# Performance work log

Hardware: AMD Instinct MI355X
Metric: run time of the kernel (lower is better)

Reference implementation:

```python
import jax, jax.numpy as jnp
import numpy as np

N = 50000          # num_nodes
IN_CH = 128
H = 32             # hidden_channels
D = 2              # stalk dimension d (= final_d, add_lp=add_hp=False)
LAYERS = 4
EU = 400000        # undirected edges
E = 2 * EU         # directed edges (both orientations)
OUT = 32


def setup_inputs() -> dict:
    key = jax.random.key(0)
    ks = jax.random.split(key, 12)
    # undirected random graph; directed edge list holds both orientations so that
    # the reverse of directed edge e is e + EU (mod E)
    u = jax.random.randint(ks[0], (EU,), 0, N)
    v = jax.random.randint(ks[1], (EU,), 0, N)
    edge_index = jnp.stack([jnp.concatenate([u, v]), jnp.concatenate([v, u])]).astype(jnp.int64)
    x = jax.random.normal(ks[2], (N, IN_CH), dtype=jnp.float32)
    W1 = jax.random.normal(ks[3], (H * D, IN_CH), dtype=jnp.float32) / np.sqrt(IN_CH)
    b1 = jax.random.normal(ks[4], (H * D,), dtype=jnp.float32) * 0.01
    W_sheaf = jax.random.normal(ks[5], (LAYERS, D, 2 * D * H), dtype=jnp.float32) / np.sqrt(2 * D * H)
    # lin_left initialised to identity in the module; keep near-identity
    W_left = jnp.tile(jnp.eye(D, dtype=jnp.float32), (LAYERS, 1, 1)) \
        + 0.01 * jax.random.normal(ks[6], (LAYERS, D, D), dtype=jnp.float32)
    W_right = jax.random.normal(ks[7], (LAYERS, H, H), dtype=jnp.float32) / np.sqrt(H)
    eps = jnp.zeros((LAYERS, D, 1), dtype=jnp.float32) + 0.01 * jax.random.normal(ks[8], (LAYERS, D, 1), dtype=jnp.float32)
    W2 = jax.random.normal(ks[9], (OUT, D * H), dtype=jnp.float32) / np.sqrt(D * H)
    b2 = jax.random.normal(ks[10], (OUT,), dtype=jnp.float32) * 0.01
    return {"x": x, "edge_index": edge_index, "W1": W1, "b1": b1, "W_sheaf": W_sheaf,
            "W_left": W_left, "W_right": W_right, "eps": eps, "W2": W2, "b2": b2}


def reference(x, edge_index, W1, b1, W_sheaf, W_left, W_right, eps, W2, b2):
    # eval mode: dropouts are no-ops; diagnostic energies/eigsh omitted (no effect on output)
    n = x.shape[0]
    d = W_left.shape[-1]
    h = W_right.shape[-1]
    src, dst = edge_index[0], edge_index[1]
    e = src.shape[0]
    rev = (jnp.arange(e) + e // 2) % e  # reverse directed edge

    x = jax.nn.elu(x @ W1.T + b1)      # [N, d*h]
    x = x.reshape(n * d, h)
    x0 = x

    for l in range(W_left.shape[0]):
        # --- sheaf learner: tanh(Linear([x_i || x_j])), diag maps F: [E, d] ---
        xn = x.reshape(n, d * h)
        feat = jnp.concatenate([xn[src], xn[dst]], axis=-1)   # [E, 2dh]
        F = jnp.tanh(feat @ W_sheaf[l].T)                     # [E, d]
        Fr = F[rev]
        # --- diag sheaf Laplacian (normalised, augmented: D_hat = D + I) ---
        Dg = jax.ops.segment_sum(F * F, src, num_segments=n)  # [N, d] diagonal blocks
        dinv = jax.lax.rsqrt(Dg + 1.0)
        diagw = Dg * dinv * dinv                              # [N, d]
        offw = -F * Fr * dinv[src] * dinv[dst]                # [E, d]
        # --- left weights: view x^T as [h, N, d], mix stalk dim ---
        xt = x.T.reshape(h, n, d) @ W_left[l].T
        x = xt.reshape(h, n * d).T
        # --- right weights ---
        x = x @ W_right[l].T
        # --- spmm: y = L x ---
        x3 = x.reshape(n, d, h)
        y = diagw[:, :, None] * x3 \
            + jax.ops.segment_sum(offw[:, :, None] * x3[dst], src, num_segments=n)
        x = jax.nn.elu(y.reshape(n * d, h))
        # --- epsilon-gated residual ---
        coeff = jnp.tile(1.0 + jnp.tanh(eps[l]), (n, 1))      # [N*d, 1]
        x0 = coeff * x0 - x
        x = x0

    return x.reshape(n, d * h) @ W2.T + b2
```

## Files before the change

kernel.cpp:

```cpp
#include <hip/hip_runtime.h>
#include <math.h>

#define INCH 128
#define DH 64
#define H  32
#define D  2
#define LAYERS 4
#define OUTC 32

typedef __fp16 half4 __attribute__((ext_vector_type(4)));
typedef float  f32x4 __attribute__((ext_vector_type(4)));

__device__ __forceinline__ float eluf(float v) { return v > 0.f ? v : expm1f(v); }

__device__ __forceinline__ float ftanh(float x) {
    float xc = fminf(9.0f, fmaxf(-9.0f, x));
    float e2 = __builtin_amdgcn_exp2f(xc * 2.885390081777927f);
    return (e2 - 1.0f) * __builtin_amdgcn_rcpf(e2 + 1.0f);
}

__global__ void k_prep(const float* __restrict__ W1, const float* __restrict__ W2,
                       const float* __restrict__ Wleft, const float* __restrict__ Wright,
                       __fp16* __restrict__ W1h, __fp16* __restrict__ W2h,
                       __fp16* __restrict__ Mlrh) {
    int idx = blockIdx.x * blockDim.x + threadIdx.x;
    if (idx < DH * INCH) {
        W1h[idx] = (__fp16)W1[idx];
    } else if (idx < DH * INCH + OUTC * DH) {
        int i = idx - DH * INCH;
        W2h[i] = (__fp16)W2[i];
    } else if (idx < DH * INCH + OUTC * DH + LAYERS * DH * DH) {
        int i = idx - DH * INCH - OUTC * DH;
        int l = i >> 12;
        int r = i & 4095;
        int row = r >> 6;
        int col = r & 63;
        int sp = row >> 5, c = row & 31;
        int s  = col >> 5, cp = col & 31;
        Mlrh[i] = (__fp16)(Wleft[l * 4 + sp * 2 + s] * Wright[l * 1024 + c * 32 + cp]);
    }
}

__global__ void k_hist(const int* __restrict__ src, int* __restrict__ deg, int E) {
    int e = blockIdx.x * blockDim.x + threadIdx.x;
    if (e < E) atomicAdd(&deg[src[e]], 1);
}

__global__ void k_bsum(const int* __restrict__ deg, int* __restrict__ bsum, int N) {
    int b = blockIdx.x, t = threadIdx.x;
    int lane = t & 63, wid = t >> 6;
    int base = b * 1024 + t * 4;
    int s = 0;
    #pragma unroll
    for (int i = 0; i < 4; ++i) {
        int idx = base + i;
        if (idx < N) s += deg[idx];
    }
    #pragma unroll
    for (int ofs = 32; ofs; ofs >>= 1) s += __shfl_xor(s, ofs);
    __shared__ int ws[4];
    if (lane == 0) ws[wid] = s;
    __syncthreads();
    if (t == 0) bsum[b] = ws[0] + ws[1] + ws[2] + ws[3];
}

__global__ void k_scan_small(int* __restrict__ bsum, int B) {
    int lane = threadIdx.x;
    int carry = 0;
    for (int base = 0; base < B; base += 64) {
        int i = base + lane;
        int v = (i < B) ? bsum[i] : 0;
        int incl = v;
        #pragma unroll
        for (int ofs = 1; ofs < 64; ofs <<= 1) {
            int tt = __shfl_up(incl, ofs);
            if (lane >= ofs) incl += tt;
        }
        if (i < B) bsum[i] = carry + incl - v;
        carry += __shfl(incl, 63);
    }
}

__global__ void k_scan_final(const int* __restrict__ deg, const int* __restrict__ bsum,
                             int* __restrict__ rowptr, int* __restrict__ cur, int N) {
    int b = blockIdx.x, t = threadIdx.x;
    int lane = t & 63, wid = t >> 6;
    int base = b * 1024 + t * 4;
    int v[4];
    int s = 0;
    #pragma unroll
    for (int i = 0; i < 4; ++i) {
        int idx = base + i;
        v[i] = (idx < N) ? deg[idx] : 0;
        s += v[i];
    }
    int incl = s;
    #pragma unroll
    for (int ofs = 1; ofs < 64; ofs <<= 1) {
        int tt = __shfl_up(incl, ofs);
        if (lane >= ofs) incl += tt;
    }
    __shared__ int ws[4];
    if (lane == 63) ws[wid] = incl;
    __syncthreads();
    int woff = 0;
    for (int k = 0; k < wid; ++k) woff += ws[k];
    int excl = bsum[b] + woff + incl - s;
    #pragma unroll
    for (int i = 0; i < 4; ++i) {
        int idx = base + i;
        if (idx < N) { rowptr[idx] = excl; cur[idx] = excl; }
        excl += v[i];
        if (idx == N - 1) rowptr[N] = excl;
    }
}

__global__ void k_scatter(const int* __restrict__ src, const int* __restrict__ dst,
                          int* __restrict__ cur, int* __restrict__ csr_dst, int E) {
    int e = blockIdx.x * blockDim.x + threadIdx.x;
    if (e >= E) return;
    int pos = atomicAdd(&cur[src[e]], 1);
    csr_dst[pos] = dst[e];
}


__global__ __launch_bounds__(256) void k_mlp1(const float* __restrict__ xin,
                                              const __fp16* __restrict__ W1h,
                                              const float* __restrict__ b1,
                                              float* __restrict__ X, int N) {
    __shared__ float xs[16 * INCH];
    __shared__ __fp16 wsh[DH * 132];
    int t = threadIdx.x;
    int node0 = blockIdx.x * 16;
    for (int i = t; i < 16 * INCH / 4; i += 256) {
        int r = i >> 5, c = (i & 31) * 4;
        int node = node0 + r;
        f32x4 v = (node < N) ? __builtin_nontemporal_load((const f32x4*)(xin + (size_t)node * INCH + c))
                             : (f32x4){0.f, 0.f, 0.f, 0.f};
        *(f32x4*)&xs[r * INCH + c] = v;
    }
    for (int i = t; i < DH * INCH / 4; i += 256) {
        int r = i >> 5, c = (i & 31) * 4;
        *(uint2*)&wsh[r * 132 + c] = ((const uint2*)W1h)[i];
    }
    __syncthreads();
    int w = t >> 6, lane = t & 63;
    int oc0 = w * 16;
    int rr = lane & 15, g = lane >> 4;
    f32x4 acc = {0.f, 0.f, 0.f, 0.f};
    #pragma unroll
    for (int ks = 0; ks < INCH / 16; ++ks) {
        f32x4 xv = *(const f32x4*)&xs[rr * INCH + ks * 16 + g * 4];
        half4 af = {(__fp16)xv.x, (__fp16)xv.y, (__fp16)xv.z, (__fp16)xv.w};
        half4 bf = *(const half4*)&wsh[(oc0 + rr) * 132 + ks * 16 + g * 4];
        acc = __builtin_amdgcn_mfma_f32_16x16x16f16(af, bf, acc, 0, 0, 0);
    }
    int oc = oc0 + rr;
    float bb = b1[oc];
    #pragma unroll
    for (int r = 0; r < 4; ++r) {
        int node = node0 + g * 4 + r;
        if (node < N) X[(size_t)node * DH + oc] = eluf(acc[r] + bb);
    }
}

__global__ void k_pq(const float* __restrict__ X, const float* __restrict__ Wsl,
                     float4* __restrict__ PQ4, int N) {
    int wid = (blockIdx.x * blockDim.x + threadIdx.x) >> 6;
    int lane = threadIdx.x & 63;
    if (wid >= N) return;
    float x = X[(size_t)wid * DH + lane];
    float p0 = x * Wsl[lane];
    float q0 = x * Wsl[64 + lane];
    float p1 = x * Wsl[128 + lane];
    float q1 = x * Wsl[192 + lane];
    #pragma unroll
    for (int ofs = 32; ofs; ofs >>= 1) {
        p0 += __shfl_xor(p0, ofs);
        q0 += __shfl_xor(q0, ofs);
        p1 += __shfl_xor(p1, ofs);
        q1 += __shfl_xor(q1, ofs);
    }
    if (lane == 0) PQ4[wid] = make_float4(p0, p1, q0, q1);
}

__global__ __launch_bounds__(256) void k_lr(const float* __restrict__ X,
                                            const __fp16* __restrict__ Mlrh_l,
                                            __fp16* __restrict__ XW0h,
                                            __fp16* __restrict__ XW1h, int N) {
    __shared__ float xs[16 * DH];
    __shared__ __fp16 mlh[DH * 68];
    int t = threadIdx.x;
    int node0 = blockIdx.x * 16;
    for (int i = t; i < 16 * DH / 4; i += 256) {
        int r = i >> 4, c = (i & 15) * 4;
        int node = node0 + r;
        f32x4 v = (node < N) ? __builtin_nontemporal_load((const f32x4*)(X + (size_t)node * DH + c))
                             : (f32x4){0.f, 0.f, 0.f, 0.f};
        *(f32x4*)&xs[r * DH + c] = v;
    }
    for (int i = t; i < DH * DH / 4; i += 256) {
        int r = i >> 4, c = (i & 15) * 4;
        *(uint2*)&mlh[r * 68 + c] = ((const uint2*)Mlrh_l)[i];
    }
    __syncthreads();
    int w = t >> 6, lane = t & 63;
    int oc0 = w * 16;
    int rr = lane & 15, g = lane >> 4;
    f32x4 acc = {0.f, 0.f, 0.f, 0.f};
    #pragma unroll
    for (int ks = 0; ks < DH / 16; ++ks) {
        f32x4 xv = *(const f32x4*)&xs[rr * DH + ks * 16 + g * 4];
        half4 af = {(__fp16)xv.x, (__fp16)xv.y, (__fp16)xv.z, (__fp16)xv.w};
        half4 bf = *(const half4*)&mlh[(oc0 + rr) * 68 + ks * 16 + g * 4];
        acc = __builtin_amdgcn_mfma_f32_16x16x16f16(af, bf, acc, 0, 0, 0);
    }
    int oc = oc0 + rr;
    int sp = oc >> 5, c = oc & 31;
    __fp16* __restrict__ XWs = sp ? XW1h : XW0h;
    #pragma unroll
    for (int r = 0; r < 4; ++r) {
        int node = node0 + g * 4 + r;
        if (node < N) XWs[(size_t)node * H + c] = (__fp16)acc[r];
    }
}

__global__ __launch_bounds__(256) void k_out(const float* __restrict__ X,
                                             const __fp16* __restrict__ W2h,
                                             const float* __restrict__ b2,
                                             float* __restrict__ out, int N) {
    __shared__ float xs[32 * DH];
    __shared__ __fp16 w2s[OUTC * 68];
    int t = threadIdx.x;
    int node0 = blockIdx.x * 32;
    for (int i = t; i < 32 * DH / 4; i += 256) {
        int r = i >> 4, c = (i & 15) * 4;
        int node = node0 + r;
        f32x4 v = (node < N) ? __builtin_nontemporal_load((const f32x4*)(X + (size_t)node * DH + c))
                             : (f32x4){0.f, 0.f, 0.f, 0.f};
        *(f32x4*)&xs[r * DH + c] = v;
    }
    for (int i = t; i < OUTC * DH / 4; i += 256) {
        int r = i >> 4, c = (i & 15) * 4;
        *(uint2*)&w2s[r * 68 + c] = ((const uint2*)W2h)[i];
    }
    __syncthreads();
    int w = t >> 6, lane = t & 63;
    int nt = w >> 1;
    int oc0 = (w & 1) * 16;
    int rr = lane & 15, g = lane >> 4;
    f32x4 acc = {0.f, 0.f, 0.f, 0.f};
    #pragma unroll
    for (int ks = 0; ks < DH / 16; ++ks) {
        f32x4 xv = *(const f32x4*)&xs[(nt * 16 + rr) * DH + ks * 16 + g * 4];
        half4 af = {(__fp16)xv.x, (__fp16)xv.y, (__fp16)xv.z, (__fp16)xv.w};
        half4 bf = *(const half4*)&w2s[(oc0 + rr) * 68 + ks * 16 + g * 4];
        acc = __builtin_amdgcn_mfma_f32_16x16x16f16(af, bf, acc, 0, 0, 0);
    }
    int oc = oc0 + rr;
    float bb = b2[oc];
    #pragma unroll
    for (int r = 0; r < 4; ++r) {
        int node = node0 + nt * 16 + g * 4 + r;
        if (node < N) out[(size_t)node * OUTC + oc] = acc[r] + bb;
    }
}


__global__ void k_dg(const float4* __restrict__ PQ4, const int* __restrict__ rowptr,
                     const int* __restrict__ csr_dst, float4* __restrict__ DGI, int N) {
    int wid = (blockIdx.x * blockDim.x + threadIdx.x) >> 6;
    int lane = threadIdx.x & 63;
    int nn = lane >> 4, sub = lane & 15;
    int node = wid * 4 + nn;
    if (node >= N) return;
    float4 pqu = PQ4[node];
    int pos = rowptr[node], end = rowptr[node + 1];
    float sx = 0.f, sy = 0.f;
    for (int i = pos + sub; i < end; i += 16) {
        int v = __builtin_nontemporal_load(csr_dst + i);
        float4 pqv = PQ4[v];
        float fx = ftanh(pqu.x + pqv.z);
        float fy = ftanh(pqu.y + pqv.w);
        sx += fx * fx;
        sy += fy * fy;
    }
    #pragma unroll
    for (int ofs = 8; ofs; ofs >>= 1) {
        sx += __shfl_xor(sx, ofs);
        sy += __shfl_xor(sy, ofs);
    }
    if (sub == 0) {
        float i0 = 1.f / (sx + 1.f), i1 = 1.f / (sy + 1.f);
        DGI[node] = make_float4(sqrtf(i0), sqrtf(i1), sx * i0, sy * i1);
    }
}

__global__ void k_spmm_fin_pq(const __fp16* __restrict__ XW0h, const __fp16* __restrict__ XW1h,
                              const float4* __restrict__ PQ4, const int* __restrict__ rowptr,
                              const int* __restrict__ csr_dst, const float4* __restrict__ DGI,
                              const float* __restrict__ eps_l, const float* __restrict__ Wsn,
                              float* __restrict__ X, float4* __restrict__ PQ4n, int N) {
    int wid = (blockIdx.x * blockDim.x + threadIdx.x) >> 6;
    int lane = threadIdx.x & 63;
    if (wid >= N) return;
    int q = lane >> 3;
    int m = lane & 7;
    float4 pqu = PQ4[wid];
    float4 giu = DGI[wid];
    float dinv0 = giu.x, dinv1 = giu.y;
    int pos = rowptr[wid], end = rowptr[wid + 1];

    float a0x = 0.f, a0y = 0.f, a0z = 0.f, a0w = 0.f;
    float a1x = 0.f, a1y = 0.f, a1z = 0.f, a1w = 0.f;

    for (int chunk = pos; chunk < end; chunk += 64) {
        int myidx = chunk + lane;
        int dmy = 0;
        float w0my = 0.f, w1my = 0.f;
        if (myidx < end) {
            dmy = __builtin_nontemporal_load(csr_dst + myidx);
            float4 pqd = PQ4[dmy];
            float4 gid = DGI[dmy];
            float ff0 = ftanh(pqu.x + pqd.z), fb0 = ftanh(pqd.x + pqu.z);
            float ff1 = ftanh(pqu.y + pqd.w), fb1 = ftanh(pqd.y + pqu.w);
            w0my = -ff0 * fb0 * dinv0 * gid.x;
            w1my = -ff1 * fb1 * dinv1 * gid.y;
        }
        int lim = end - chunk; if (lim > 64) lim = 64;
        for (int b = 0; b < lim; b += 8) {
            int sl = b + q;
            int d      = __shfl(dmy, sl);
            float w0e  = __shfl(w0my, sl);
            float w1e  = __shfl(w1my, sl);
            half4 g0 = *(const half4*)(XW0h + (size_t)d * H + m * 4);
            half4 g1 = *(const half4*)(XW1h + (size_t)d * H + m * 4);
            a0x += w0e * (float)g0.x; a0y += w0e * (float)g0.y;
            a0z += w0e * (float)g0.z; a0w += w0e * (float)g0.w;
            a1x += w1e * (float)g1.x; a1y += w1e * (float)g1.y;
            a1z += w1e * (float)g1.z; a1w += w1e * (float)g1.w;
        }
    }
    #pragma unroll
    for (int ofs = 8; ofs <= 32; ofs <<= 1) {
        a0x += __shfl_xor(a0x, ofs); a0y += __shfl_xor(a0y, ofs);
        a0z += __shfl_xor(a0z, ofs); a0w += __shfl_xor(a0w, ofs);
        a1x += __shfl_xor(a1x, ofs); a1y += __shfl_xor(a1y, ofs);
        a1z += __shfl_xor(a1z, ofs); a1w += __shfl_xor(a1w, ofs);
    }
    if (q == 0) {
        float diag0 = giu.z;
        float diag1 = giu.w;
        half4 xw0 = *(const half4*)(XW0h + (size_t)wid * H + m * 4);
        half4 xw1 = *(const half4*)(XW1h + (size_t)wid * H + m * 4);
        size_t b0 = (size_t)wid * DH + m * 4;
        size_t b1 = b0 + 32;
        float coeff0 = 1.f + tanhf(eps_l[0]);
        float coeff1 = 1.f + tanhf(eps_l[1]);
        f32x4 xo0 = __builtin_nontemporal_load((const f32x4*)(X + b0));
        f32x4 xo1 = __builtin_nontemporal_load((const f32x4*)(X + b1));
        f32x4 xn0, xn1;
        xn0.x = coeff0 * xo0.x - eluf(diag0 * (float)xw0.x + a0x);
        xn0.y = coeff0 * xo0.y - eluf(diag0 * (float)xw0.y + a0y);
        xn0.z = coeff0 * xo0.z - eluf(diag0 * (float)xw0.z + a0z);
        xn0.w = coeff0 * xo0.w - eluf(diag0 * (float)xw0.w + a0w);
        xn1.x = coeff1 * xo1.x - eluf(diag1 * (float)xw1.x + a1x);
        xn1.y = coeff1 * xo1.y - eluf(diag1 * (float)xw1.y + a1y);
        xn1.z = coeff1 * xo1.z - eluf(diag1 * (float)xw1.z + a1z);
        xn1.w = coeff1 * xo1.w - eluf(diag1 * (float)xw1.w + a1w);
        __builtin_nontemporal_store(xn0, (f32x4*)(X + b0));
        __builtin_nontemporal_store(xn1, (f32x4*)(X + b1));
        if (Wsn) {
            f32x4 wa0 = *(const f32x4*)(Wsn + m * 4);
            f32x4 wa1 = *(const f32x4*)(Wsn + 32 + m * 4);
            f32x4 wb0 = *(const f32x4*)(Wsn + 64 + m * 4);
            f32x4 wb1 = *(const f32x4*)(Wsn + 96 + m * 4);
            f32x4 wc0 = *(const f32x4*)(Wsn + 128 + m * 4);
            f32x4 wc1 = *(const f32x4*)(Wsn + 160 + m * 4);
            f32x4 wd0 = *(const f32x4*)(Wsn + 192 + m * 4);
            f32x4 wd1 = *(const f32x4*)(Wsn + 224 + m * 4);
            float p0 = xn0.x * wa0.x + xn0.y * wa0.y + xn0.z * wa0.z + xn0.w * wa0.w
                     + xn1.x * wa1.x + xn1.y * wa1.y + xn1.z * wa1.z + xn1.w * wa1.w;
            float q0 = xn0.x * wb0.x + xn0.y * wb0.y + xn0.z * wb0.z + xn0.w * wb0.w
                     + xn1.x * wb1.x + xn1.y * wb1.y + xn1.z * wb1.z + xn1.w * wb1.w;
            float p1 = xn0.x * wc0.x + xn0.y * wc0.y + xn0.z * wc0.z + xn0.w * wc0.w
                     + xn1.x * wc1.x + xn1.y * wc1.y + xn1.z * wc1.z + xn1.w * wc1.w;
            float q1 = xn0.x * wd0.x + xn0.y * wd0.y + xn0.z * wd0.z + xn0.w * wd0.w
                     + xn1.x * wd1.x + xn1.y * wd1.y + xn1.z * wd1.z + xn1.w * wd1.w;
            #pragma unroll
            for (int ofs = 1; ofs < 8; ofs <<= 1) {
                p0 += __shfl_xor(p0, ofs);
                q0 += __shfl_xor(q0, ofs);
                p1 += __shfl_xor(p1, ofs);
                q1 += __shfl_xor(q1, ofs);
            }
            if (m == 0) PQ4n[wid] = make_float4(p0, p1, q0, q1);
        }
    }
}

extern "C" void kernel_launch(void* const* d_in, const int* in_sizes, int n_in,
                              void* d_out, int out_size, void* d_ws, size_t ws_size,
                              hipStream_t stream) {
    const float* xin    = (const float*)d_in[0];
    const int*   ei     = (const int*)d_in[1];
    const float* W1     = (const float*)d_in[2];
    const float* b1     = (const float*)d_in[3];
    const float* Wsheaf = (const float*)d_in[4];
    const float* Wleft  = (const float*)d_in[5];
    const float* Wright = (const float*)d_in[6];
    const float* eps    = (const float*)d_in[7];
    const float* W2     = (const float*)d_in[8];
    const float* b2     = (const float*)d_in[9];
    float* out = (float*)d_out;

    int N = in_sizes[0] / INCH;
    int E = in_sizes[1] / 2;
    const int* src = ei;
    const int* dst = ei + E;

    size_t off = 0;
    auto alloc = [&](size_t nbytes) {
        char* p = (char*)d_ws + off;
        off += (nbytes + 255) & ~(size_t)255;
        return p;
    };
    float*   X       = (float*)alloc((size_t)N * DH * 4);
    __fp16*  XW0h    = (__fp16*)alloc((size_t)N * H * 2);
    __fp16*  XW1h    = (__fp16*)alloc((size_t)N * H * 2);
    float4*  DGI     = (float4*)alloc((size_t)N * 16);
    float4*  PQ4a    = (float4*)alloc((size_t)N * 16);
    float4*  PQ4b    = (float4*)alloc((size_t)N * 16);
    int*     deg     = (int*)alloc((size_t)N * 4);
    int*     rowptr  = (int*)alloc(((size_t)N + 1) * 4);
    int*     cur     = (int*)alloc((size_t)N * 4);
    int*     csr_dst = (int*)alloc((size_t)E * 4);
    int*     bsum    = (int*)alloc(4096);
    __fp16*  W1h     = (__fp16*)alloc((size_t)DH * INCH * 2);
    __fp16*  W2h     = (__fp16*)alloc((size_t)OUTC * DH * 2);
    __fp16*  Mlrh    = (__fp16*)alloc((size_t)LAYERS * DH * DH * 2);

    int B = (N + 1023) / 1024;

    int prep_total = DH * INCH + OUTC * DH + LAYERS * DH * DH;
    k_prep<<<(prep_total + 255) / 256, 256, 0, stream>>>(W1, W2, Wleft, Wright, W1h, W2h, Mlrh);
    hipMemsetAsync(deg, 0, (size_t)N * sizeof(int), stream);
    k_hist<<<(E + 255) / 256, 256, 0, stream>>>(src, deg, E);
    k_bsum<<<B, 256, 0, stream>>>(deg, bsum, N);
    k_scan_small<<<1, 64, 0, stream>>>(bsum, B);
    k_scan_final<<<B, 256, 0, stream>>>(deg, bsum, rowptr, cur, N);
    k_scatter<<<(E + 255) / 256, 256, 0, stream>>>(src, dst, cur, csr_dst, E);

    k_mlp1<<<(N + 15) / 16, 256, 0, stream>>>(xin, W1h, b1, X, N);
    k_pq<<<(N + 3) / 4, 256, 0, stream>>>(X, Wsheaf, PQ4a, N);

    float4* PQcur = PQ4a;
    float4* PQnext = PQ4b;
    for (int l = 0; l < LAYERS; ++l) {
        k_dg<<<(N + 15) / 16, 256, 0, stream>>>(PQcur, rowptr, csr_dst, DGI, N);
        k_lr<<<(N + 15) / 16, 256, 0, stream>>>(X, Mlrh + (size_t)l * DH * DH, XW0h, XW1h, N);
        const float* Wsn = (l + 1 < LAYERS) ? (Wsheaf + (l + 1) * 2 * INCH) : nullptr;
        k_spmm_fin_pq<<<(N + 3) / 4, 256, 0, stream>>>(XW0h, XW1h, PQcur, rowptr, csr_dst,
                                                       DGI, eps + l * 2, Wsn, X, PQnext, N);
        float4* tmp = PQcur; PQcur = PQnext; PQnext = tmp;
    }

    k_out<<<(N + 31) / 32, 256, 0, stream>>>(X, W2h, b2, out, N);
}
```

Measured before the change: 408.3 us.

## Precompute fp16 edge weights and split SpMM into two column-half passes

Adds a kernel that computes the per-edge Laplacian weights once per layer and stores them as fp16 pairs in CSR order. The SpMM is split into two launches, each gathering a 32-half-wide slice of the transformed features: 16 columns from each stalk dimension, interleaved so every gather is a single 64-byte row. The aim is to shrink the gathered working set per pass so it stays in cache and to drop the tanh work from the SpMM. In exchange, edge indices and weights are read twice, there are extra launches, the next-layer sheaf projection goes through a partial buffer, and the weights lose precision by being stored in fp16.

```diff
diff --git a/kernel.cpp b/kernel.cpp
--- a/kernel.cpp
+++ b/kernel.cpp
@@ -9,6 +9,7 @@
 #define OUTC 32
 
 typedef __fp16 half4 __attribute__((ext_vector_type(4)));
+typedef __fp16 half2h __attribute__((ext_vector_type(2)));
 typedef float  f32x4 __attribute__((ext_vector_type(4)));
 
 __device__ __forceinline__ float eluf(float v) { return v > 0.f ? v : expm1f(v); }
@@ -186,8 +187,8 @@
 
 __global__ __launch_bounds__(256) void k_lr(const float* __restrict__ X,
                                             const __fp16* __restrict__ Mlrh_l,
-                                            __fp16* __restrict__ XW0h,
-                                            __fp16* __restrict__ XW1h, int N) {
+                                            __fp16* __restrict__ XWA,
+                                            __fp16* __restrict__ XWB, int N) {
     __shared__ float xs[16 * DH];
     __shared__ __fp16 mlh[DH * 68];
     int t = threadIdx.x;
@@ -217,11 +218,12 @@
     }
     int oc = oc0 + rr;
     int sp = oc >> 5, c = oc & 31;
-    __fp16* __restrict__ XWs = sp ? XW1h : XW0h;
+    __fp16* __restrict__ XWs = (c >= 16) ? XWB : XWA;
+    int cidx = sp * 16 + (c & 15);
     #pragma unroll
     for (int r = 0; r < 4; ++r) {
         int node = node0 + g * 4 + r;
-        if (node < N) XWs[(size_t)node * H + c] = (__fp16)acc[r];
+        if (node < N) XWs[(size_t)node * 32 + cidx] = (__fp16)acc[r];
     }
 }
 
@@ -296,97 +298,83 @@
     }
 }
 
-__global__ void k_spmm_fin_pq(const __fp16* __restrict__ XW0h, const __fp16* __restrict__ XW1h,
-                              const float4* __restrict__ PQ4, const int* __restrict__ rowptr,
-                              const int* __restrict__ csr_dst, const float4* __restrict__ DGI,
+__global__ void k_we(const float4* __restrict__ PQ4, const float4* __restrict__ DGI,
+                     const int* __restrict__ rowptr, const int* __restrict__ csr_dst,
+                     half2h* __restrict__ csr_w, int N) {
+    int wid = (blockIdx.x * blockDim.x + threadIdx.x) >> 6;
+    int lane = threadIdx.x & 63;
+    int nn = lane >> 4, sub = lane & 15;
+    int node = wid * 4 + nn;
+    if (node >= N) return;
+    float4 pqu = PQ4[node];
+    float4 giu = DGI[node];
+    int pos = rowptr[node], end = rowptr[node + 1];
+    for (int i = pos + sub; i < end; i += 16) {
+        int v = __builtin_nontemporal_load(csr_dst + i);
+        float4 pqv = PQ4[v];
+        float4 giv = DGI[v];
+        float ff0 = ftanh(pqu.x + pqv.z), fb0 = ftanh(pqv.x + pqu.z);
+        float ff1 = ftanh(pqu.y + pqv.w), fb1 = ftanh(pqv.y + pqu.w);
+        float w0 = -ff0 * fb0 * giu.x * giv.x;
+        float w1 = -ff1 * fb1 * giu.y * giv.y;
+        csr_w[i] = (half2h){(__fp16)w0, (__fp16)w1};
+    }
+}
+
+template <int HALF>
+__global__ void k_spmm_fin_pq(const __fp16* __restrict__ XWh,
+                              const int* __restrict__ rowptr, const int* __restrict__ csr_dst,
+                              const unsigned* __restrict__ csr_wu, const float4* __restrict__ DGI,
                               const float* __restrict__ eps_l, const float* __restrict__ Wsn,
-                              float* __restrict__ X, float4* __restrict__ PQ4n, int N) {
+                              float* __restrict__ X, float4* __restrict__ PQpart,
+                              float4* __restrict__ PQ4n, int N) {
     int wid = (blockIdx.x * blockDim.x + threadIdx.x) >> 6;
     int lane = threadIdx.x & 63;
     if (wid >= N) return;
     int q = lane >> 3;
     int m = lane & 7;
-    float4 pqu = PQ4[wid];
-    float4 giu = DGI[wid];
-    float dinv0 = giu.x, dinv1 = giu.y;
     int pos = rowptr[wid], end = rowptr[wid + 1];
 
-    float a0x = 0.f, a0y = 0.f, a0z = 0.f, a0w = 0.f;
-    float a1x = 0.f, a1y = 0.f, a1z = 0.f, a1w = 0.f;
-
-    for (int chunk = pos; chunk < end; chunk += 64) {
-        int myidx = chunk + lane;
-        int dmy = 0;
-        float w0my = 0.f, w1my = 0.f;
-        if (myidx < end) {
-            dmy = __builtin_nontemporal_load(csr_dst + myidx);
-            float4 pqd = PQ4[dmy];
-            float4 gid = DGI[dmy];
-            float ff0 = ftanh(pqu.x + pqd.z), fb0 = ftanh(pqd.x + pqu.z);
-            float ff1 = ftanh(pqu.y + pqd.w), fb1 = ftanh(pqd.y + pqu.w);
-            w0my = -ff0 * fb0 * dinv0 * gid.x;
-            w1my = -ff1 * fb1 * dinv1 * gid.y;
-        }
-        int lim = end - chunk; if (lim > 64) lim = 64;
-        for (int b = 0; b < lim; b += 8) {
-            int sl = b + q;
-            int d      = __shfl(dmy, sl);
-            float w0e  = __shfl(w0my, sl);
-            float w1e  = __shfl(w1my, sl);
-            half4 g0 = *(const half4*)(XW0h + (size_t)d * H + m * 4);
-            half4 g1 = *(const half4*)(XW1h + (size_t)d * H + m * 4);
-            a0x += w0e * (float)g0.x; a0y += w0e * (float)g0.y;
-            a0z += w0e * (float)g0.z; a0w += w0e * (float)g0.w;
-            a1x += w1e * (float)g1.x; a1y += w1e * (float)g1.y;
-            a1z += w1e * (float)g1.z; a1w += w1e * (float)g1.w;
-        }
+    float ax = 0.f, ay = 0.f, az = 0.f, aw = 0.f;
+    for (int idx = pos + q; idx < end; idx += 8) {
+        int d = __builtin_nontemporal_load(csr_dst + idx);
+        unsigned wraw = __builtin_nontemporal_load(csr_wu + idx);
+        half2h wv;
+        __builtin_memcpy(&wv, &wraw, 4);
+        float wgt = (m < 4) ? (float)wv.x : (float)wv.y;
+        half4 g = *(const half4*)(XWh + (size_t)d * 32 + m * 4);
+        ax += wgt * (float)g.x; ay += wgt * (float)g.y;
+        az += wgt * (float)g.z; aw += wgt * (float)g.w;
     }
     #pragma unroll
     for (int ofs = 8; ofs <= 32; ofs <<= 1) {
-        a0x += __shfl_xor(a0x, ofs); a0y += __shfl_xor(a0y, ofs);
-        a0z += __shfl_xor(a0z, ofs); a0w += __shfl_xor(a0w, ofs);
-        a1x += __shfl_xor(a1x, ofs); a1y += __shfl_xor(a1y, ofs);
-        a1z += __shfl_xor(a1z, ofs); a1w += __shfl_xor(a1w, ofs);
+        ax += __shfl_xor(ax, ofs); ay += __shfl_xor(ay, ofs);
+        az += __shfl_xor(az, ofs); aw += __shfl_xor(aw, ofs);
     }
     if (q == 0) {
-        float diag0 = giu.z;
-        float diag1 = giu.w;
-        half4 xw0 = *(const half4*)(XW0h + (size_t)wid * H + m * 4);
-        half4 xw1 = *(const half4*)(XW1h + (size_t)wid * H + m * 4);
-        size_t b0 = (size_t)wid * DH + m * 4;
-        size_t b1 = b0 + 32;
-        float coeff0 = 1.f + tanhf(eps_l[0]);
-        float coeff1 = 1.f + tanhf(eps_l[1]);
-        f32x4 xo0 = __builtin_nontemporal_load((const f32x4*)(X + b0));
-        f32x4 xo1 = __builtin_nontemporal_load((const f32x4*)(X + b1));
-        f32x4 xn0, xn1;
-        xn0.x = coeff0 * xo0.x - eluf(diag0 * (float)xw0.x + a0x);
-        xn0.y = coeff0 * xo0.y - eluf(diag0 * (float)xw0.y + a0y);
-        xn0.z = coeff0 * xo0.z - eluf(diag0 * (float)xw0.z + a0z);
-        xn0.w = coeff0 * xo0.w - eluf(diag0 * (float)xw0.w + a0w);
-        xn1.x = coeff1 * xo1.x - eluf(diag1 * (float)xw1.x + a1x);
-        xn1.y = coeff1 * xo1.y - eluf(diag1 * (float)xw1.y + a1y);
-        xn1.z = coeff1 * xo1.z - eluf(diag1 * (float)xw1.z + a1z);
-        xn1.w = coeff1 * xo1.w - eluf(diag1 * (float)xw1.w + a1w);
-        __builtin_nontemporal_store(xn0, (f32x4*)(X + b0));
-        __builtin_nontemporal_store(xn1, (f32x4*)(X + b1));
+        float4 giu = DGI[wid];
+        int s = (m >= 4);
+        float diag = s ? giu.w : giu.z;
+        half4 xw = *(const half4*)(XWh + (size_t)wid * 32 + m * 4);
+        int coffs = s * 32 + HALF * 16 + (m & 3) * 4;
+        size_t bx = (size_t)wid * DH + coffs;
+        float coeff = 1.f + tanhf(eps_l[s]);
+        f32x4 xo = __builtin_nontemporal_load((const f32x4*)(X + bx));
+        f32x4 xn;
+        xn.x = coeff * xo.x - eluf(diag * (float)xw.x + ax);
+        xn.y = coeff * xo.y - eluf(diag * (float)xw.y + ay);
+        xn.z = coeff * xo.z - eluf(diag * (float)xw.z + az);
+        xn.w = coeff * xo.w - eluf(diag * (float)xw.w + aw);
+        __builtin_nontemporal_store(xn, (f32x4*)(X + bx));
         if (Wsn) {
-            f32x4 wa0 = *(const f32x4*)(Wsn + m * 4);
-            f32x4 wa1 = *(const f32x4*)(Wsn + 32 + m * 4);
-            f32x4 wb0 = *(const f32x4*)(Wsn + 64 + m * 4);
-            f32x4 wb1 = *(const f32x4*)(Wsn + 96 + m * 4);
-            f32x4 wc0 = *(const f32x4*)(Wsn + 128 + m * 4);
-            f32x4 wc1 = *(const f32x4*)(Wsn + 160 + m * 4);
-            f32x4 wd0 = *(const f32x4*)(Wsn + 192 + m * 4);
-            f32x4 wd1 = *(const f32x4*)(Wsn + 224 + m * 4);
-            float p0 = xn0.x * wa0.x + xn0.y * wa0.y + xn0.z * wa0.z + xn0.w * wa0.w
-                     + xn1.x * wa1.x + xn1.y * wa1.y + xn1.z * wa1.z + xn1.w * wa1.w;
-            float q0 = xn0.x * wb0.x + xn0.y * wb0.y + xn0.z * wb0.z + xn0.w * wb0.w
-                     + xn1.x * wb1.x + xn1.y * wb1.y + xn1.z * wb1.z + xn1.w * wb1.w;
-            float p1 = xn0.x * wc0.x + xn0.y * wc0.y + xn0.z * wc0.z + xn0.w * wc0.w
-                     + xn1.x * wc1.x + xn1.y * wc1.y + xn1.z * wc1.z + xn1.w * wc1.w;
-            float q1 = xn0.x * wd0.x + xn0.y * wd0.y + xn0.z * wd0.z + xn0.w * wd0.w
-                     + xn1.x * wd1.x + xn1.y * wd1.y + xn1.z * wd1.z + xn1.w * wd1.w;
+            f32x4 wpa = *(const f32x4*)(Wsn + coffs);
+            f32x4 wqa = *(const f32x4*)(Wsn + 64 + coffs);
+            f32x4 wpb = *(const f32x4*)(Wsn + 128 + coffs);
+            f32x4 wqb = *(const f32x4*)(Wsn + 192 + coffs);
+            float p0 = xn.x * wpa.x + xn.y * wpa.y + xn.z * wpa.z + xn.w * wpa.w;
+            float q0 = xn.x * wqa.x + xn.y * wqa.y + xn.z * wqa.z + xn.w * wqa.w;
+            float p1 = xn.x * wpb.x + xn.y * wpb.y + xn.z * wpb.z + xn.w * wpb.w;
+            float q1 = xn.x * wqb.x + xn.y * wqb.y + xn.z * wqb.z + xn.w * wqb.w;
             #pragma unroll
             for (int ofs = 1; ofs < 8; ofs <<= 1) {
                 p0 += __shfl_xor(p0, ofs);
@@ -394,7 +382,14 @@
                 p1 += __shfl_xor(p1, ofs);
                 q1 += __shfl_xor(q1, ofs);
             }
-            if (m == 0) PQ4n[wid] = make_float4(p0, p1, q0, q1);
+            if (m == 0) {
+                if (HALF == 0) {
+                    PQpart[wid] = make_float4(p0, p1, q0, q1);
+                } else {
+                    float4 pp = PQpart[wid];
+                    PQ4n[wid] = make_float4(pp.x + p0, pp.y + p1, pp.z + q0, pp.w + q1);
+                }
+            }
         }
     }
 }
@@ -426,15 +421,17 @@
         return p;
     };
     float*   X       = (float*)alloc((size_t)N * DH * 4);
-    __fp16*  XW0h    = (__fp16*)alloc((size_t)N * H * 2);
-    __fp16*  XW1h    = (__fp16*)alloc((size_t)N * H * 2);
+    __fp16*  XWA     = (__fp16*)alloc((size_t)N * 32 * 2);
+    __fp16*  XWB     = (__fp16*)alloc((size_t)N * 32 * 2);
     float4*  DGI     = (float4*)alloc((size_t)N * 16);
     float4*  PQ4a    = (float4*)alloc((size_t)N * 16);
     float4*  PQ4b    = (float4*)alloc((size_t)N * 16);
+    float4*  PQpart  = (float4*)alloc((size_t)N * 16);
     int*     deg     = (int*)alloc((size_t)N * 4);
     int*     rowptr  = (int*)alloc(((size_t)N + 1) * 4);
     int*     cur     = (int*)alloc((size_t)N * 4);
     int*     csr_dst = (int*)alloc((size_t)E * 4);
+    half2h*  csr_w   = (half2h*)alloc((size_t)E * 4);
     int*     bsum    = (int*)alloc(4096);
     __fp16*  W1h     = (__fp16*)alloc((size_t)DH * INCH * 2);
     __fp16*  W2h     = (__fp16*)alloc((size_t)OUTC * DH * 2);
@@ -458,10 +455,13 @@
     float4* PQnext = PQ4b;
     for (int l = 0; l < LAYERS; ++l) {
         k_dg<<<(N + 15) / 16, 256, 0, stream>>>(PQcur, rowptr, csr_dst, DGI, N);
-        k_lr<<<(N + 15) / 16, 256, 0, stream>>>(X, Mlrh + (size_t)l * DH * DH, XW0h, XW1h, N);
+        k_we<<<(N + 15) / 16, 256, 0, stream>>>(PQcur, DGI, rowptr, csr_dst, csr_w, N);
+        k_lr<<<(N + 15) / 16, 256, 0, stream>>>(X, Mlrh + (size_t)l * DH * DH, XWA, XWB, N);
         const float* Wsn = (l + 1 < LAYERS) ? (Wsheaf + (l + 1) * 2 * INCH) : nullptr;
-        k_spmm_fin_pq<<<(N + 3) / 4, 256, 0, stream>>>(XW0h, XW1h, PQcur, rowptr, csr_dst,
-                                                       DGI, eps + l * 2, Wsn, X, PQnext, N);
+        k_spmm_fin_pq<0><<<(N + 3) / 4, 256, 0, stream>>>(XWA, rowptr, csr_dst, (const unsigned*)csr_w,
+                                                          DGI, eps + l * 2, Wsn, X, PQpart, PQnext, N);
+        k_spmm_fin_pq<1><<<(N + 3) / 4, 256, 0, stream>>>(XWB, rowptr, csr_dst, (const unsigned*)csr_w,
+                                                          DGI, eps + l * 2, Wsn, X, PQpart, PQnext, N);
         float4* tmp = PQcur; PQcur = PQnext; PQnext = tmp;
     }
 
```

Measured after the change: 560.1 us. 1.37x slower.
